# Kernel tuning notes

Measured on AMD Instinct MI355X. Metric: run time of the kernel, lower is better.

Reference implementation:

```python
import jax, jax.numpy as jnp
import numpy as np

L_COORD = 5.0
L_NOOBJ = 0.5
NUM_B = 2


def setup_inputs() -> dict:
    key = jax.random.key(0)
    ks = jax.random.split(key, 6)
    N, S, Bb, C = 4096, 14, NUM_B, 20
    pred_cls = jax.random.uniform(ks[0], (N, S, S, C), dtype=jnp.float32)
    pred_response = jax.random.uniform(ks[1], (N, S, S, Bb), dtype=jnp.float32)
    pred_bboxes = jax.random.uniform(ks[2], (N, S, S, Bb * 4), dtype=jnp.float32)
    label_cls = jax.random.uniform(ks[3], (N, S, S, C), dtype=jnp.float32)
    # binary objectness per cell, tiled over the B response channels
    obj_bit = jax.random.randint(ks[4], (N, S, S), 0, 2).astype(jnp.float32)
    label_response = jnp.tile(obj_bit[..., None], (1, 1, 1, Bb))
    label_bboxes = jax.random.uniform(ks[5], (N, S, S, Bb * 4), dtype=jnp.float32)
    return {
        "pred_cls": pred_cls,
        "pred_response": pred_response,
        "pred_bboxes": pred_bboxes,
        "label_cls": label_cls,
        "label_response": label_response,
        "label_bboxes": label_bboxes,
    }


def _to_corners(p):
    # p: [..., B, 4] with (x, y, sqrt_w, sqrt_h); corners via w = sqrt_w**2
    xy = p[..., 0:2]
    half_wh = 0.5 * p[..., 2:4] ** 2
    return jnp.concatenate([xy - half_wh, xy + half_wh], axis=-1)


def _iou_elementwise(b1, b2):
    # b1, b2: [..., 4] corner boxes; elementwise IoU (matches compute_iou with N==M broadcast)
    lt = jnp.maximum(b1[..., 0:2], b2[..., 0:2])
    rb = jnp.minimum(b1[..., 2:4], b2[..., 2:4])
    wh = jnp.maximum(rb - lt, 0.0)
    inter = wh[..., 0] * wh[..., 1]
    a1 = (b1[..., 2] - b1[..., 0]) * (b1[..., 3] - b1[..., 1])
    a2 = (b2[..., 2] - b2[..., 0]) * (b2[..., 3] - b2[..., 1])
    return inter / (a1 + a2 - inter)


def reference(pred_cls, pred_response, pred_bboxes, label_cls, label_response, label_bboxes):
    N, S = pred_response.shape[0], pred_response.shape[1]
    Bb = NUM_B
    bs = jnp.float32(N)

    obj = (label_response[..., 0] > 0).astype(pred_cls.dtype)      # [N,S,S]
    noobj = (label_response[..., 0] < 1).astype(pred_cls.dtype)    # [N,S,S]

    # no-object containment loss over all B channels
    nobj_loss = jnp.sum(noobj[..., None] * (pred_response - label_response) ** 2) / bs

    # class loss on object cells
    cls_loss = jnp.sum(obj[..., None] * (pred_cls - label_cls) ** 2) / bs

    # per-box IoU between matching pred/target boxes j (dense, masked later)
    pb = pred_bboxes.reshape(N, S, S, Bb, 4)
    tb = label_bboxes.reshape(N, S, S, Bb, 4)
    iou = _iou_elementwise(_to_corners(tb), _to_corners(pb))  # [N,S,S,B]

    max_iou = jnp.max(iou, axis=-1)                            # [N,S,S]
    best = jnp.argmax(iou, axis=-1)                            # [N,S,S]

    best_p = jnp.take_along_axis(pb, best[..., None, None], axis=3)[:, :, :, 0, :]  # [N,S,S,4]
    best_t = jnp.take_along_axis(tb, best[..., None, None], axis=3)[:, :, :, 0, :]
    pred_resp_best = jnp.take_along_axis(pred_response, best[..., None], axis=-1)[..., 0]
    label_resp_best = jnp.take_along_axis(label_response, best[..., None], axis=-1)[..., 0]

    # coordinate loss on the responsible box (xy + sqrt-wh terms)
    coord_loss = jnp.sum(obj[..., None] * (best_p - best_t) ** 2) / bs

    # max_iou is detached in the original (.data)
    max_iou_d = jax.lax.stop_gradient(max_iou)
    pobj_loss = jnp.sum(obj * (pred_resp_best - max_iou_d) ** 2) / bs
    iou_loss = jnp.sum(obj * (max_iou_d - label_resp_best) ** 2) / bs

    # [offset, cls, pObj, nObj, iou]
    return jnp.stack([L_COORD * coord_loss, cls_loss, pobj_loss, L_NOOBJ * nobj_loss, iou_loss])
```

## Files before the change

kernel.cpp:

```cpp
#include <hip/hip_runtime.h>


constexpr int NCELL  = 4096 * 14 * 14;
constexpr int TPB    = 256;
constexpr int BLOCKS = 784;
constexpr int ITERS  = 4;
constexpr int STRIDE = BLOCKS * TPB;

constexpr float INV_BS  = 1.0f / 4096.0f;
constexpr float L_COORD = 5.0f;
constexpr float L_NOOBJ = 0.5f;

__device__ __forceinline__ float iou_corners(float4 t, float4 p) {
    float thx = 0.5f * t.z * t.z;
    float thy = 0.5f * t.w * t.w;
    float t_l = t.x - thx, t_t = t.y - thy;
    float t_r = t.x + thx, t_b = t.y + thy;
    float phx = 0.5f * p.z * p.z;
    float phy = 0.5f * p.w * p.w;
    float p_l = p.x - phx, p_t = p.y - phy;
    float p_r = p.x + phx, p_b = p.y + phy;
    float ltx = fmaxf(t_l, p_l), lty = fmaxf(t_t, p_t);
    float rbx = fminf(t_r, p_r), rby = fminf(t_b, p_b);
    float wx = fmaxf(rbx - ltx, 0.0f), wy = fmaxf(rby - lty, 0.0f);
    float inter = wx * wy;
    float a1 = (t_r - t_l) * (t_b - t_t);
    float a2 = (p_r - p_l) * (p_b - p_t);
    return inter / (a1 + a2 - inter);
}

__global__ __launch_bounds__(TPB) void yolo_loss_main(
    const float* __restrict__ pred_cls,
    const float* __restrict__ pred_resp,
    const float* __restrict__ pred_bb,
    const float* __restrict__ label_cls,
    const float* __restrict__ label_resp,
    const float* __restrict__ label_bb,
    float* __restrict__ ws)
{
    const int tid0 = blockIdx.x * TPB + threadIdx.x;

    float coord = 0.0f, cls = 0.0f, pobj = 0.0f, nobj = 0.0f, iouL = 0.0f;

    float2 lr[ITERS], pr[ITERS];
    #pragma unroll
    for (int it = 0; it < ITERS; ++it) {
        int cell = tid0 + it * STRIDE;
        lr[it] = *reinterpret_cast<const float2*>(label_resp + (size_t)cell * 2);
        pr[it] = *reinterpret_cast<const float2*>(pred_resp  + (size_t)cell * 2);
    }

    #pragma unroll
    for (int it = 0; it < ITERS; ++it) {
        int cell = tid0 + it * STRIDE;
        bool obj = lr[it].x > 0.0f;

        if (!obj) {
            float d0 = pr[it].x - lr[it].x, d1 = pr[it].y - lr[it].y;
            nobj += d0 * d0 + d1 * d1;
        } else {
            const float4* pc = reinterpret_cast<const float4*>(pred_cls  + (size_t)cell * 20);
            const float4* lc = reinterpret_cast<const float4*>(label_cls + (size_t)cell * 20);
            #pragma unroll
            for (int k = 0; k < 5; ++k) {
                float4 a = pc[k], b = lc[k];
                float dx = a.x - b.x, dy = a.y - b.y, dz = a.z - b.z, dw = a.w - b.w;
                cls += dx * dx + dy * dy + dz * dz + dw * dw;
            }

            const float4* pbp = reinterpret_cast<const float4*>(pred_bb  + (size_t)cell * 8);
            const float4* tbp = reinterpret_cast<const float4*>(label_bb + (size_t)cell * 8);
            float4 pb0 = pbp[0], pb1 = pbp[1];
            float4 tb0 = tbp[0], tb1 = tbp[1];

            float iou0 = iou_corners(tb0, pb0);
            float iou1 = iou_corners(tb1, pb1);

            bool best1 = iou1 > iou0;
            float max_iou = fmaxf(iou0, iou1);

            float4 bp = best1 ? pb1 : pb0;
            float4 bt = best1 ? tb1 : tb0;
            float dx = bp.x - bt.x, dy = bp.y - bt.y, dz = bp.z - bt.z, dw = bp.w - bt.w;
            coord += dx * dx + dy * dy + dz * dz + dw * dw;

            float pr_best = best1 ? pr[it].y : pr[it].x;
            float lr_best = best1 ? lr[it].y : lr[it].x;
            float dpo = pr_best - max_iou;
            float dio = max_iou - lr_best;
            pobj += dpo * dpo;
            iouL += dio * dio;
        }
    }

    #pragma unroll
    for (int off = 32; off > 0; off >>= 1) {
        coord += __shfl_down(coord, off);
        cls   += __shfl_down(cls,   off);
        pobj  += __shfl_down(pobj,  off);
        nobj  += __shfl_down(nobj,  off);
        iouL  += __shfl_down(iouL,  off);
    }

    __shared__ float part[4][5];
    int wave = threadIdx.x >> 6;
    int lane = threadIdx.x & 63;
    if (lane == 0) {
        part[wave][0] = coord;
        part[wave][1] = cls;
        part[wave][2] = pobj;
        part[wave][3] = nobj;
        part[wave][4] = iouL;
    }
    __syncthreads();
    if (threadIdx.x == 0) {
        float* w = ws + (size_t)blockIdx.x * 8;
        w[0] = part[0][0] + part[1][0] + part[2][0] + part[3][0];
        w[1] = part[0][1] + part[1][1] + part[2][1] + part[3][1];
        w[2] = part[0][2] + part[1][2] + part[2][2] + part[3][2];
        w[3] = part[0][3] + part[1][3] + part[2][3] + part[3][3];
        w[4] = part[0][4] + part[1][4] + part[2][4] + part[3][4];
    }
}

__global__ __launch_bounds__(TPB) void yolo_loss_finish(
    const float* __restrict__ ws,
    float* __restrict__ out)
{
    float s0 = 0.0f, s1 = 0.0f, s2 = 0.0f, s3 = 0.0f, s4 = 0.0f;
    for (int b = threadIdx.x; b < BLOCKS; b += TPB) {
        const float* w = ws + (size_t)b * 8;
        s0 += w[0]; s1 += w[1]; s2 += w[2]; s3 += w[3]; s4 += w[4];
    }
    #pragma unroll
    for (int off = 32; off > 0; off >>= 1) {
        s0 += __shfl_down(s0, off);
        s1 += __shfl_down(s1, off);
        s2 += __shfl_down(s2, off);
        s3 += __shfl_down(s3, off);
        s4 += __shfl_down(s4, off);
    }
    __shared__ float part[4][5];
    int wave = threadIdx.x >> 6;
    int lane = threadIdx.x & 63;
    if (lane == 0) {
        part[wave][0] = s0; part[wave][1] = s1; part[wave][2] = s2;
        part[wave][3] = s3; part[wave][4] = s4;
    }
    __syncthreads();
    if (threadIdx.x == 0) {
        float t0 = part[0][0] + part[1][0] + part[2][0] + part[3][0];
        float t1 = part[0][1] + part[1][1] + part[2][1] + part[3][1];
        float t2 = part[0][2] + part[1][2] + part[2][2] + part[3][2];
        float t3 = part[0][3] + part[1][3] + part[2][3] + part[3][3];
        float t4 = part[0][4] + part[1][4] + part[2][4] + part[3][4];
        out[0] = L_COORD * INV_BS * t0;
        out[1] = INV_BS * t1;
        out[2] = INV_BS * t2;
        out[3] = L_NOOBJ * INV_BS * t3;
        out[4] = INV_BS * t4;
    }
}

extern "C" void kernel_launch(void* const* d_in, const int* in_sizes, int n_in,
                              void* d_out, int out_size, void* d_ws, size_t ws_size,
                              hipStream_t stream) {
    const float* pred_cls   = (const float*)d_in[0];
    const float* pred_resp  = (const float*)d_in[1];
    const float* pred_bb    = (const float*)d_in[2];
    const float* label_cls  = (const float*)d_in[3];
    const float* label_resp = (const float*)d_in[4];
    const float* label_bb   = (const float*)d_in[5];
    float* ws  = (float*)d_ws;
    float* out = (float*)d_out;

    yolo_loss_main<<<BLOCKS, TPB, 0, stream>>>(
        pred_cls, pred_resp, pred_bb, label_cls, label_resp, label_bb, ws);
    yolo_loss_finish<<<1, TPB, 0, stream>>>(ws, out);
}
```

Before: 200.1 us.

## Use one cell per thread with unconditional loads and branchless masking

Replaces the grid-stride loop (784 blocks, 4 cells per thread) with one cell per thread over NCELL/TPB blocks. Every thread now loads all class and bbox data up front and applies the objectness mask as a multiply instead of branching. This removes divergent, load-dependent branches so more independent loads are in flight. The cost is that every cell's class and box data is read, including no-object cells that the old branch skipped, and the finish kernel now reduces many more block partials.

After: 206.7 us. 1.03x slower.

```diff
diff --git a/kernel.cpp b/kernel.cpp
--- a/kernel.cpp
+++ b/kernel.cpp
@@ -3,9 +3,7 @@
 
 constexpr int NCELL  = 4096 * 14 * 14;
 constexpr int TPB    = 256;
-constexpr int BLOCKS = 784;
-constexpr int ITERS  = 4;
-constexpr int STRIDE = BLOCKS * TPB;
+constexpr int BLOCKS = NCELL / TPB;
 
 constexpr float INV_BS  = 1.0f / 4096.0f;
 constexpr float L_COORD = 5.0f;
@@ -38,60 +36,54 @@
     const float* __restrict__ label_bb,
     float* __restrict__ ws)
 {
-    const int tid0 = blockIdx.x * TPB + threadIdx.x;
+    const int cell = blockIdx.x * TPB + threadIdx.x;
 
-    float coord = 0.0f, cls = 0.0f, pobj = 0.0f, nobj = 0.0f, iouL = 0.0f;
+    const float2 lr = *reinterpret_cast<const float2*>(label_resp + (size_t)cell * 2);
+    const float2 pr = *reinterpret_cast<const float2*>(pred_resp  + (size_t)cell * 2);
 
-    float2 lr[ITERS], pr[ITERS];
-    #pragma unroll
-    for (int it = 0; it < ITERS; ++it) {
-        int cell = tid0 + it * STRIDE;
-        lr[it] = *reinterpret_cast<const float2*>(label_resp + (size_t)cell * 2);
-        pr[it] = *reinterpret_cast<const float2*>(pred_resp  + (size_t)cell * 2);
+    const float4* pc = reinterpret_cast<const float4*>(pred_cls  + (size_t)cell * 20);
+    const float4* lc = reinterpret_cast<const float4*>(label_cls + (size_t)cell * 20);
+    float4 a0 = pc[0], a1 = pc[1], a2 = pc[2], a3 = pc[3], a4 = pc[4];
+    float4 b0 = lc[0], b1 = lc[1], b2 = lc[2], b3 = lc[3], b4 = lc[4];
+
+    const float4* pbp = reinterpret_cast<const float4*>(pred_bb  + (size_t)cell * 8);
+    const float4* tbp = reinterpret_cast<const float4*>(label_bb + (size_t)cell * 8);
+    float4 pb0 = pbp[0], pb1 = pbp[1];
+    float4 tb0 = tbp[0], tb1 = tbp[1];
+
+    const float obj  = (lr.x > 0.0f) ? 1.0f : 0.0f;
+    const float nob  = 1.0f - obj;
+
+    float d0 = pr.x - lr.x, d1 = pr.y - lr.y;
+    float nobj = nob * (d0 * d0 + d1 * d1);
+
+    float c = 0.0f;
+    {
+        float dx, dy, dz, dw;
+        dx = a0.x-b0.x; dy = a0.y-b0.y; dz = a0.z-b0.z; dw = a0.w-b0.w; c += dx*dx+dy*dy+dz*dz+dw*dw;
+        dx = a1.x-b1.x; dy = a1.y-b1.y; dz = a1.z-b1.z; dw = a1.w-b1.w; c += dx*dx+dy*dy+dz*dz+dw*dw;
+        dx = a2.x-b2.x; dy = a2.y-b2.y; dz = a2.z-b2.z; dw = a2.w-b2.w; c += dx*dx+dy*dy+dz*dz+dw*dw;
+        dx = a3.x-b3.x; dy = a3.y-b3.y; dz = a3.z-b3.z; dw = a3.w-b3.w; c += dx*dx+dy*dy+dz*dz+dw*dw;
+        dx = a4.x-b4.x; dy = a4.y-b4.y; dz = a4.z-b4.z; dw = a4.w-b4.w; c += dx*dx+dy*dy+dz*dz+dw*dw;
     }
+    float cls = obj * c;
 
-    #pragma unroll
-    for (int it = 0; it < ITERS; ++it) {
-        int cell = tid0 + it * STRIDE;
-        bool obj = lr[it].x > 0.0f;
+    float iou0 = iou_corners(tb0, pb0);
+    float iou1 = iou_corners(tb1, pb1);
+    bool best1 = iou1 > iou0;
+    float max_iou = fmaxf(iou0, iou1);
 
-        if (!obj) {
-            float d0 = pr[it].x - lr[it].x, d1 = pr[it].y - lr[it].y;
-            nobj += d0 * d0 + d1 * d1;
-        } else {
-            const float4* pc = reinterpret_cast<const float4*>(pred_cls  + (size_t)cell * 20);
-            const float4* lc = reinterpret_cast<const float4*>(label_cls + (size_t)cell * 20);
-            #pragma unroll
-            for (int k = 0; k < 5; ++k) {
-                float4 a = pc[k], b = lc[k];
-                float dx = a.x - b.x, dy = a.y - b.y, dz = a.z - b.z, dw = a.w - b.w;
-                cls += dx * dx + dy * dy + dz * dz + dw * dw;
-            }
+    float4 bp = best1 ? pb1 : pb0;
+    float4 bt = best1 ? tb1 : tb0;
+    float ex = bp.x - bt.x, ey = bp.y - bt.y, ez = bp.z - bt.z, ew = bp.w - bt.w;
+    float coord = obj * (ex * ex + ey * ey + ez * ez + ew * ew);
 
-            const float4* pbp = reinterpret_cast<const float4*>(pred_bb  + (size_t)cell * 8);
-            const float4* tbp = reinterpret_cast<const float4*>(label_bb + (size_t)cell * 8);
-            float4 pb0 = pbp[0], pb1 = pbp[1];
-            float4 tb0 = tbp[0], tb1 = tbp[1];
-
-            float iou0 = iou_corners(tb0, pb0);
-            float iou1 = iou_corners(tb1, pb1);
-
-            bool best1 = iou1 > iou0;
-            float max_iou = fmaxf(iou0, iou1);
-
-            float4 bp = best1 ? pb1 : pb0;
-            float4 bt = best1 ? tb1 : tb0;
-            float dx = bp.x - bt.x, dy = bp.y - bt.y, dz = bp.z - bt.z, dw = bp.w - bt.w;
-            coord += dx * dx + dy * dy + dz * dz + dw * dw;
-
-            float pr_best = best1 ? pr[it].y : pr[it].x;
-            float lr_best = best1 ? lr[it].y : lr[it].x;
-            float dpo = pr_best - max_iou;
-            float dio = max_iou - lr_best;
-            pobj += dpo * dpo;
-            iouL += dio * dio;
-        }
-    }
+    float pr_best = best1 ? pr.y : pr.x;
+    float lr_best = best1 ? lr.y : lr.x;
+    float dpo = pr_best - max_iou;
+    float dio = max_iou - lr_best;
+    float pobj = obj * dpo * dpo;
+    float iouL = obj * dio * dio;
 
     #pragma unroll
     for (int off = 32; off > 0; off >>= 1) {
```

## Flatten loss into coalesced per-float4 streaming with lane-pair IoU exchange

Applied to the files above, without the earlier changes.

Replaces the per-cell thread mapping with a flat mapping where each thread streams one float4 of class data and one box per iteration, so global loads are fully coalesced instead of strided by 80 or 32 bytes per cell. Branches on objectness become multiplicative masks, and the best-box choice is made by exchanging IoU between adjacent lanes with a shuffle. The grid grows to one thread per cell (3136 blocks) with fewer iterations each. The cost is reading every class element even for no-object cells and an extra label_resp gather per class float4.

Measured after the change: 203.0 us. About the same (+1.4%).

```diff
diff --git a/kernel.cpp b/kernel.cpp
--- a/kernel.cpp
+++ b/kernel.cpp
@@ -1,11 +1,12 @@
 #include <hip/hip_runtime.h>
 
 
-constexpr int NCELL  = 4096 * 14 * 14;
-constexpr int TPB    = 256;
-constexpr int BLOCKS = 784;
-constexpr int ITERS  = 4;
-constexpr int STRIDE = BLOCKS * TPB;
+constexpr int NCELL    = 4096 * 14 * 14;
+constexpr int TPB      = 256;
+constexpr int BLOCKS   = NCELL / TPB;
+constexpr int NTHREADS = NCELL;
+constexpr int CLS_IT   = 5;
+constexpr int BOX_IT   = 2;
 
 constexpr float INV_BS  = 1.0f / 4096.0f;
 constexpr float L_COORD = 5.0f;
@@ -38,59 +39,50 @@
     const float* __restrict__ label_bb,
     float* __restrict__ ws)
 {
-    const int tid0 = blockIdx.x * TPB + threadIdx.x;
+    const int tid = blockIdx.x * TPB + threadIdx.x;
 
     float coord = 0.0f, cls = 0.0f, pobj = 0.0f, nobj = 0.0f, iouL = 0.0f;
 
-    float2 lr[ITERS], pr[ITERS];
+    const float4* pc4 = reinterpret_cast<const float4*>(pred_cls);
+    const float4* lc4 = reinterpret_cast<const float4*>(label_cls);
     #pragma unroll
-    for (int it = 0; it < ITERS; ++it) {
-        int cell = tid0 + it * STRIDE;
-        lr[it] = *reinterpret_cast<const float2*>(label_resp + (size_t)cell * 2);
-        pr[it] = *reinterpret_cast<const float2*>(pred_resp  + (size_t)cell * 2);
+    for (int j = 0; j < CLS_IT; ++j) {
+        unsigned i4 = (unsigned)(j * NTHREADS + tid);
+        float4 a = pc4[i4];
+        float4 b = lc4[i4];
+        unsigned cell = i4 / 5u;
+        float o = (label_resp[(size_t)cell * 2] > 0.0f) ? 1.0f : 0.0f;
+        float dx = a.x - b.x, dy = a.y - b.y, dz = a.z - b.z, dw = a.w - b.w;
+        cls += o * (dx * dx + dy * dy + dz * dz + dw * dw);
     }
 
+    const float4* pb4 = reinterpret_cast<const float4*>(pred_bb);
+    const float4* tb4 = reinterpret_cast<const float4*>(label_bb);
     #pragma unroll
-    for (int it = 0; it < ITERS; ++it) {
-        int cell = tid0 + it * STRIDE;
-        bool obj = lr[it].x > 0.0f;
+    for (int j = 0; j < BOX_IT; ++j) {
+        int bi = j * NTHREADS + tid;
+        float4 p = pb4[bi];
+        float4 t = tb4[bi];
+        float prv = pred_resp[bi];
+        float lrv = label_resp[bi];
 
-        if (!obj) {
-            float d0 = pr[it].x - lr[it].x, d1 = pr[it].y - lr[it].y;
-            nobj += d0 * d0 + d1 * d1;
-        } else {
-            const float4* pc = reinterpret_cast<const float4*>(pred_cls  + (size_t)cell * 20);
-            const float4* lc = reinterpret_cast<const float4*>(label_cls + (size_t)cell * 20);
-            #pragma unroll
-            for (int k = 0; k < 5; ++k) {
-                float4 a = pc[k], b = lc[k];
-                float dx = a.x - b.x, dy = a.y - b.y, dz = a.z - b.z, dw = a.w - b.w;
-                cls += dx * dx + dy * dy + dz * dz + dw * dw;
-            }
+        float iou   = iou_corners(t, p);
+        float iou_o = __shfl_xor(iou, 1);
+        bool  is_b1 = (bi & 1);
+        bool  win   = is_b1 ? (iou > iou_o) : (iou >= iou_o);
+        float mx    = fmaxf(iou, iou_o);
 
-            const float4* pbp = reinterpret_cast<const float4*>(pred_bb  + (size_t)cell * 8);
-            const float4* tbp = reinterpret_cast<const float4*>(label_bb + (size_t)cell * 8);
-            float4 pb0 = pbp[0], pb1 = pbp[1];
-            float4 tb0 = tbp[0], tb1 = tbp[1];
+        float obj = (lrv > 0.0f) ? 1.0f : 0.0f;
+        float dr  = prv - lrv;
+        nobj += (1.0f - obj) * dr * dr;
 
-            float iou0 = iou_corners(tb0, pb0);
-            float iou1 = iou_corners(tb1, pb1);
-
-            bool best1 = iou1 > iou0;
-            float max_iou = fmaxf(iou0, iou1);
-
-            float4 bp = best1 ? pb1 : pb0;
-            float4 bt = best1 ? tb1 : tb0;
-            float dx = bp.x - bt.x, dy = bp.y - bt.y, dz = bp.z - bt.z, dw = bp.w - bt.w;
-            coord += dx * dx + dy * dy + dz * dz + dw * dw;
-
-            float pr_best = best1 ? pr[it].y : pr[it].x;
-            float lr_best = best1 ? lr[it].y : lr[it].x;
-            float dpo = pr_best - max_iou;
-            float dio = max_iou - lr_best;
-            pobj += dpo * dpo;
-            iouL += dio * dio;
-        }
+        float wm = win ? obj : 0.0f;
+        float ex = p.x - t.x, ey = p.y - t.y, ez = p.z - t.z, ew = p.w - t.w;
+        coord += wm * (ex * ex + ey * ey + ez * ez + ew * ew);
+        float dpo = prv - mx;
+        float dio = mx - lrv;
+        pobj += wm * dpo * dpo;
+        iouL += wm * dio * dio;
     }
 
     #pragma unroll
```
